# Kernel optimization log

Measured on AMD Instinct MI355X. Metric: run time of the kernel, lower is better.

Reference implementation:

```python
import jax, jax.numpy as jnp
import numpy as np

MUL = 32      # multiplicity of each irrep type: 32x0e + 32x1o (dim = 32 + 96 = 128)
NSPEC = 10
NGRAPH = 16
EPS = 1e-5


def _split(x):
    # x: [N, 128] -> scalars [N, 32], vectors [N, 32, 3]
    return x[:, :MUL], x[:, MUL:].reshape(x.shape[0], MUL, 3)


def _cat(s, v):
    return jnp.concatenate([s, v.reshape(v.shape[0], MUL * 3)], axis=1)


def _irreps_linear(s, v, w0, w1, b0=None):
    # e3nn o3.Linear: per-irrep-type multiplicity mixing, /sqrt(fan_in), bias on scalars only
    inv = 1.0 / np.sqrt(MUL)
    s2 = s @ w0 * inv
    if b0 is not None:
        s2 = s2 + b0
    v2 = jnp.einsum('nuc,uw->nwc', v, w1) * inv
    return s2, v2


def _tensor_product(s1, v1, s2, v2, w000, w110, w011, w101):
    # SeparateWeightTensorProduct with per-path internal weights, lmax=1 paths:
    #   0e x 0e -> 0e, 1o x 1o -> 0e (CG = delta/sqrt(3)), 0e x 1o -> 1o, 1o x 0e -> 1o
    inv = 1.0 / np.sqrt(MUL * MUL)
    half = 1.0 / np.sqrt(2.0)  # two paths feed each output irrep
    out0 = (jnp.einsum('nu,nv,uvw->nw', s1, s2, w000)
            + jnp.einsum('nuc,nvc,uvw->nw', v1, v2, w110) / np.sqrt(3.0)) * (inv * half)
    out1 = (jnp.einsum('nu,nvc,uvw->nwc', s1, v2, w011)
            + jnp.einsum('nuc,nv,uvw->nwc', v1, s2, w101)) * (inv * half)
    return out0, out1


def _e3_layer_norm(s, v, batch, ln_w0, ln_b0, ln_w1):
    # per-graph equivariant layer norm: subtract mean on scalars, RMS-normalize each irrep field
    ones = jnp.ones(batch.shape, s.dtype)
    cnt = jnp.maximum(jax.ops.segment_sum(ones, batch, NGRAPH), 1.0)
    mean = jax.ops.segment_sum(s.sum(-1), batch, NGRAPH) / (cnt * MUL)
    s = s - mean[batch][:, None]
    n2s = jax.ops.segment_sum((s * s).sum(-1), batch, NGRAPH) / (cnt * MUL)
    s = s * jax.lax.rsqrt(n2s + EPS)[batch][:, None] * ln_w0 + ln_b0
    n2v = jax.ops.segment_sum((v * v).sum((-1, -2)), batch, NGRAPH) / (cnt * MUL)
    v = v * jax.lax.rsqrt(n2v + EPS)[batch][:, None, None] * ln_w1[None, :, None]
    return s, v


def setup_inputs() -> dict:
    key = jax.random.key(0)
    ks = jax.random.split(key, 24)
    N, B = 50000, 2
    rn = lambda k, sh: jax.random.normal(k, sh, dtype=jnp.float32)
    inp = {
        'node_feats_hidden': rn(ks[0], (B, N, MUL * 4)),
        'node_feats_up': rn(ks[1], (N, MUL * 4)),
        'hl_w0': rn(ks[2], (B, MUL, MUL)), 'hl_w1': rn(ks[3], (B, MUL, MUL)),
        'ul_w0': rn(ks[4], (B, MUL, MUL)), 'ul_w1': rn(ks[5], (B, MUL, MUL)),
        'tp_w000': rn(ks[6], (B, MUL, MUL, MUL)), 'tp_w110': rn(ks[7], (B, MUL, MUL, MUL)),
        'tp_w011': rn(ks[8], (B, MUL, MUL, MUL)), 'tp_w101': rn(ks[9], (B, MUL, MUL, MUL)),
        'lp_w0': rn(ks[10], (B, MUL, MUL)), 'lp_b0': jnp.zeros((B, MUL), jnp.float32),
        'lp_w1': rn(ks[11], (B, MUL, MUL)),
        'sc_w0': rn(ks[12], (B, MUL, NSPEC, MUL)), 'sc_w1': rn(ks[13], (B, MUL, NSPEC, MUL)),
        'ln_w0': jnp.ones((B, MUL), jnp.float32), 'ln_b0': jnp.zeros((B, MUL), jnp.float32),
        'ln_w1': jnp.ones((B, MUL), jnp.float32),
        'sk_w0': rn(ks[14], (B, MUL, MUL)), 'sk_b0': jnp.zeros((B, MUL), jnp.float32),
        'sk_w1': rn(ks[15], (B, MUL, MUL)),
        'node_species': jax.random.randint(ks[16], (N,), 0, NSPEC),
        'batch': jnp.sort(jax.random.randint(ks[17], (N,), 0, NGRAPH)),
    }
    return inp


def reference(node_feats_hidden, node_feats_up, hl_w0, hl_w1, ul_w0, ul_w1,
              tp_w000, tp_w110, tp_w011, tp_w101, lp_w0, lp_b0, lp_w1,
              sc_w0, sc_w1, ln_w0, ln_b0, ln_w1, sk_w0, sk_b0, sk_w1,
              node_species, batch):
    oh = jax.nn.one_hot(node_species, NSPEC, dtype=node_feats_up.dtype)
    inv_sc = 1.0 / np.sqrt(MUL * NSPEC)
    up = node_feats_up
    outs = []
    for b in range(node_feats_hidden.shape[0]):  # num_interactions blocks (fixed, small)
        sh, vh = _split(node_feats_hidden[b])
        su, vu = _split(up)
        shp, vhp = _irreps_linear(sh, vh, hl_w0[b], hl_w1[b])
        sup, vup = _irreps_linear(su, vu, ul_w0[b], ul_w1[b])
        z0, z1 = _tensor_product(shp, vhp, sup, vup,
                                 tp_w000[b], tp_w110[b], tp_w011[b], tp_w101[b])
        z0, z1 = _irreps_linear(z0, z1, lp_w0[b], lp_w1[b], lp_b0[b])
        # self connection: FullyConnectedTensorProduct(hidden, one-hot '10x0e', out)
        z0 = z0 + jnp.einsum('nu,nv,uvw->nw', sh, oh, sc_w0[b]) * inv_sc
        z1 = z1 + jnp.einsum('nuc,nv,uvw->nwc', vh, oh, sc_w1[b]) * inv_sc
        z0, z1 = _e3_layer_norm(z0, z1, batch, ln_w0[b], ln_b0[b], ln_w1[b])
        sk0, sk1 = _irreps_linear(sh, vh, sk_w0[b], sk_w1[b], sk_b0[b])
        out = _cat(z0 + sk0, z1 + sk1)
        outs.append(out)
        up = out  # next block consumes this block's output as node_feats_up
    return jnp.stack(outs)
```

## Files before the change

### kernel.cpp

```cpp
#include <hip/hip_runtime.h>
#include <math.h>

#define MULT 32
#define NSPEC 10
#define NGRAPH 16
#define NBANK 64
#define NCBANK 16
#define INV_SC 0.05590169943749474f
#define INV32S 0.17677669529663687f

typedef unsigned short u16;
typedef __bf16 v8bf __attribute__((ext_vector_type(8)));
typedef float v4f __attribute__((ext_vector_type(4)));
typedef unsigned int v4u_t __attribute__((ext_vector_type(4)));

__device__ __forceinline__ u16 f2bf(float f) {
    unsigned int u = __builtin_bit_cast(unsigned int, f);
    unsigned int r = u + 0x7fffu + ((u >> 16) & 1u);
    return (u16)(r >> 16);
}

__device__ __forceinline__ v8bf frag16(const u16* p) {
    return __builtin_bit_cast(v8bf, *(const v4u_t*)p);
}

#define MFMA(a, b, c) __builtin_amdgcn_mfma_f32_16x16x32_bf16(a, b, c, 0, 0, 0)

__global__ void zero_kernel(float* __restrict__ p, int n) {
    int i = blockIdx.x * 256 + threadIdx.x;
    if (i < n) p[i] = 0.0f;
}

__global__ void count_kernel(const int* __restrict__ batch, float* __restrict__ cntb, int N) {
    __shared__ int bins[NGRAPH];
    int t = threadIdx.x;
    if (t < NGRAPH) bins[t] = 0;
    __syncthreads();
    int i = blockIdx.x * 256 + t;
    if (i < N) atomicAdd(&bins[batch[i]], 1);
    __syncthreads();
    int bank = blockIdx.x & (NCBANK - 1);
    if (t < NGRAPH && bins[t] > 0) atomicAdd(&cntb[bank * NGRAPH + t], (float)bins[t]);
}

__global__ void stageA_kernel(const float* __restrict__ w000, const float* __restrict__ w110,
                              const float* __restrict__ w011, const float* __restrict__ w101,
                              const float* __restrict__ lp0, const float* __restrict__ lp1,
                              float* __restrict__ tmp1) {
    int gid = blockIdx.x * 256 + threadIdx.x;
    int tslot = gid >> 15;
    int e = gid & 32767;
    int z = e & 31;
    int uv = e >> 5;
    int b = tslot >> 2, path = tslot & 3;
    const float* W = (path == 0 ? w000 : path == 1 ? w110 : path == 2 ? w011 : w101) + b * 32768;
    const float* L = ((path == 0 || path == 1) ? lp0 : lp1) + b * 1024;
    float scale = (path == 1) ? (1.0f / (8192.0f * 1.7320508075688772f)) : (1.0f / 8192.0f);
    const float* wr = W + uv * 32;
    float acc = 0.0f;
    for (int w = 0; w < 32; ++w) acc += wr[w] * L[w * 32 + z];
    tmp1[gid] = acc * scale;
}

__global__ void stageB_kernel(const float* __restrict__ ul0, const float* __restrict__ ul1,
                              const float* __restrict__ tmp1, float* __restrict__ tmp2) {
    int gid = blockIdx.x * 256 + threadIdx.x;
    int tslot = gid >> 15;
    int e = gid & 32767;
    int z = e & 31;
    int bb = (e >> 5) & 31;
    int u = e >> 10;
    int b = tslot >> 2, path = tslot & 3;
    const float* U = ((path == 0 || path == 3) ? ul0 : ul1) + b * 1024;
    const float* in = tmp1 + (size_t)tslot * 32768 + u * 1024 + z;
    float acc = 0.0f;
    for (int v = 0; v < 32; ++v) acc += U[bb * 32 + v] * in[v * 32];
    tmp2[gid] = acc;
}

__global__ void stageC_kernel(const float* __restrict__ hl0, const float* __restrict__ hl1,
                              const float* __restrict__ tmp2, float* __restrict__ Weff) {
    int gid = blockIdx.x * 256 + threadIdx.x;
    int tslot = gid >> 15;
    int e = gid & 32767;
    int z = e & 31;
    int bb = (e >> 5) & 31;
    int a = e >> 10;
    int b = tslot >> 2, path = tslot & 3;
    const float* H = ((path == 0 || path == 2) ? hl0 : hl1) + b * 1024;
    const float* in = tmp2 + (size_t)tslot * 32768 + bb * 32 + z;
    float acc = 0.0f;
    for (int u = 0; u < 32; ++u) acc += H[a * 32 + u] * in[u * 1024];
    Weff[gid] = acc;
}

__global__ void pack_kernel(const float* __restrict__ Weff,
                            const float* __restrict__ sc_w0, const float* __restrict__ sc_w1,
                            u16* __restrict__ packs, int total) {
    int gid = blockIdx.x * 256 + threadIdx.x;
    if (gid >= total) return;
    int b = gid / 151552;
    int e = gid - b * 151552;
    float v;
    if (e < 131072) {
        int which = e >> 15;
        int e2 = e & 32767;
        int k = e2 & 31;
        int z = (e2 >> 5) & 31;
        int hi = e2 >> 10;
        int path = (which == 0) ? 0 : (which == 1) ? 2 : (which == 2) ? 3 : 1;
        int a  = (which < 2) ? k  : hi;
        int bb = (which < 2) ? hi : k;
        v = Weff[(size_t)((b * 4 + path) * 32 + a) * 1024 + bb * 32 + z];
    } else {
        int e2 = e - 131072;
        int which = e2 / 10240;
        int e3 = e2 - which * 10240;
        int s = e3 >> 10, z = (e3 >> 5) & 31, a = e3 & 31;
        const float* S = which ? sc_w1 : sc_w0;
        v = S[(size_t)b * 10240 + a * 320 + s * 32 + z] * INV_SC;
    }
    packs[gid] = f2bf(v);
}

__attribute__((amdgpu_waves_per_eu(4, 4)))
__global__ __launch_bounds__(256)
void tp_kernel(const float* __restrict__ hidden_b, const float* __restrict__ up,
               const u16* __restrict__ pk,
               const float* __restrict__ lp_b0,
               const int* __restrict__ species, const int* __restrict__ batch,
               float* __restrict__ S1b, float* __restrict__ S2b, float* __restrict__ V2b,
               float* __restrict__ zout, int N) {
    constexpr int OFF_000 = 0, OFF_011 = 32768, OFF_101 = 65536, OFF_110 = 98304;
    constexpr int OFF_SC0 = 131072, OFF_SC1 = 141312;

    __shared__ __align__(16) char smem[33792];
    __shared__ int spec_l[16];
    __shared__ int bat_l[16];
    __shared__ float gs1[NGRAPH], gs2[NGRAPH], gv2[NGRAPH];

    u16* sh_bf = (u16*)smem;
    u16* su_bf = (u16*)(smem + 1280);
    u16* vu_bf = (u16*)(smem + 2560);
    u16* vh_bf = (u16*)(smem + 6400);
    float* suT = (float*)(smem + 10240);
    float* vuT = (float*)(smem + 12288);
    float* vhT = (float*)(smem + 18432);
    float* red = (float*)smem;

    const int t = threadIdx.x;
    const int w = t >> 6, lane = t & 63, quad = lane >> 4, c16 = lane & 15;
    const int n0 = blockIdx.x * 16;
    const int nvalid = min(16, N - n0);

    if (t < NGRAPH) { gs1[t] = 0.f; gs2[t] = 0.f; gv2[t] = 0.f; }
    if (t < 16) {
        spec_l[t] = (t < nvalid) ? species[n0 + t] : -1;
        bat_l[t]  = (t < nvalid) ? batch[n0 + t] : 0;
    }
    for (int i = t; i < 2048; i += 256) {
        int n = i >> 7, col = i & 127;
        float hv = 0.f, uv = 0.f;
        if (n < nvalid) {
            hv = hidden_b[(size_t)(n0 + n) * 128 + col];
            uv = up[(size_t)(n0 + n) * 128 + col];
        }
        if (col < 32) {
            sh_bf[n * 40 + col] = f2bf(hv); su_bf[n * 40 + col] = f2bf(uv);
            suT[col * 16 + n] = uv;
        } else {
            int idx = col - 32, c = idx % 3, a = idx / 3;
            vh_bf[(c * 16 + n) * 40 + a] = f2bf(hv);
            vu_bf[(c * 16 + n) * 40 + a] = f2bf(uv);
            vhT[(c * 32 + a) * 16 + n] = hv;
            vuT[(c * 32 + a) * 16 + n] = uv;
        }
    }
    __syncthreads();

    const v4f z4 = {0.f, 0.f, 0.f, 0.f};
    v4f o0[2];
    v4f o1[3][2];
    o0[0] = z4; o0[1] = z4;
#pragma unroll
    for (int c = 0; c < 3; ++c) { o1[c][0] = z4; o1[c][1] = z4; }

    v8bf a_sh = frag16(sh_bf + c16 * 40 + quad * 8);

    {
        const u16* Wb = pk + OFF_000 + (w * 16 * 16 + c16) * 32 + quad * 8;
#pragma unroll 4
        for (int th = 0; th < 8; ++th) {
            int bb = w * 8 + th;
            v4f y = *(const v4f*)(suT + bb * 16 + quad * 4);
            v8bf bf0 = frag16(Wb + (th * 2) * 512);
            v8bf bf1 = frag16(Wb + (th * 2 + 1) * 512);
            v4f C0 = MFMA(a_sh, bf0, z4);
            v4f C1 = MFMA(a_sh, bf1, z4);
#pragma unroll
            for (int r = 0; r < 4; ++r) {
                o0[0][r] += C0[r] * y[r];
                o0[1][r] += C1[r] * y[r];
            }
        }
    }
    {
        const u16* Wb = pk + OFF_011 + (w * 16 * 16 + c16) * 32 + quad * 8;
#pragma unroll 2
        for (int th = 0; th < 8; ++th) {
            int bb = w * 8 + th;
            v8bf bf0 = frag16(Wb + (th * 2) * 512);
            v8bf bf1 = frag16(Wb + (th * 2 + 1) * 512);
            v4f C0 = MFMA(a_sh, bf0, z4);
            v4f C1 = MFMA(a_sh, bf1, z4);
#pragma unroll
            for (int c = 0; c < 3; ++c) {
                v4f y = *(const v4f*)(vuT + (c * 32 + bb) * 16 + quad * 4);
#pragma unroll
                for (int r = 0; r < 4; ++r) {
                    o1[c][0][r] += C0[r] * y[r];
                    o1[c][1][r] += C1[r] * y[r];
                }
            }
        }
    }
    {
        v8bf a_su = frag16(su_bf + c16 * 40 + quad * 8);
        const u16* Wb = pk + OFF_101 + (w * 16 * 16 + c16) * 32 + quad * 8;
#pragma unroll 2
        for (int th = 0; th < 8; ++th) {
            int aa = w * 8 + th;
            v8bf bf0 = frag16(Wb + (th * 2) * 512);
            v8bf bf1 = frag16(Wb + (th * 2 + 1) * 512);
            v4f C0 = MFMA(a_su, bf0, z4);
            v4f C1 = MFMA(a_su, bf1, z4);
#pragma unroll
            for (int c = 0; c < 3; ++c) {
                v4f y = *(const v4f*)(vhT + (c * 32 + aa) * 16 + quad * 4);
#pragma unroll
                for (int r = 0; r < 4; ++r) {
                    o1[c][0][r] += C0[r] * y[r];
                    o1[c][1][r] += C1[r] * y[r];
                }
            }
        }
    }
#pragma unroll
    for (int c = 0; c < 3; ++c) {
        v8bf av = frag16(vu_bf + (c * 16 + c16) * 40 + quad * 8);
        const u16* Wb = pk + OFF_110 + (w * 16 * 16 + c16) * 32 + quad * 8;
#pragma unroll 4
        for (int th = 0; th < 8; ++th) {
            int aa = w * 8 + th;
            v4f y = *(const v4f*)(vhT + (c * 32 + aa) * 16 + quad * 4);
            v8bf bf0 = frag16(Wb + (th * 2) * 512);
            v8bf bf1 = frag16(Wb + (th * 2 + 1) * 512);
            v4f C0 = MFMA(av, bf0, z4);
            v4f C1 = MFMA(av, bf1, z4);
#pragma unroll
            for (int r = 0; r < 4; ++r) {
                o0[0][r] += C0[r] * y[r];
                o0[1][r] += C1[r] * y[r];
            }
        }
    }
    {
        const int s0 = (w < 2) ? w * 3 : 6 + (w - 2) * 2;
        const int ns = (w < 2) ? 3 : 2;
        v8bf zf = __builtin_bit_cast(v8bf, (v4u_t){0u, 0u, 0u, 0u});
        int sp = spec_l[c16];
        for (int si = s0; si < s0 + ns; ++si) {
            bool m = (sp == si);
            v8bf ash_m = m ? a_sh : zf;
#pragma unroll
            for (int zh = 0; zh < 2; ++zh) {
                int boff = (si * 32 + zh * 16 + c16) * 32 + quad * 8;
                v8bf bf0 = frag16(pk + OFF_SC0 + boff);
                v8bf bf1 = frag16(pk + OFF_SC1 + boff);
                o0[zh] = MFMA(ash_m, bf0, o0[zh]);
#pragma unroll
                for (int c = 0; c < 3; ++c) {
                    v8bf av = frag16(vh_bf + (c * 16 + c16) * 40 + quad * 8);
                    v8bf am = m ? av : zf;
                    o1[c][zh] = MFMA(am, bf1, o1[c][zh]);
                }
            }
        }
    }

    __syncthreads();
#pragma unroll
    for (int r = 0; r < 4; ++r) {
        int n = quad * 4 + r;
        float* row = red + (w * 16 + n) * 132;
        row[c16]      = o0[0][r];
        row[16 + c16] = o0[1][r];
#pragma unroll
        for (int c = 0; c < 3; ++c) {
            row[32 + c16 * 3 + c]        = o1[c][0][r];
            row[32 + (16 + c16) * 3 + c] = o1[c][1][r];
        }
    }
    __syncthreads();
    {
        int n = t >> 4, seg = t & 15;
        v4f sa = z4, sb = z4;
#pragma unroll
        for (int ww = 0; ww < 4; ++ww) {
            const float* rp = red + (ww * 16 + n) * 132 + seg * 8;
            sa += *(const v4f*)rp;
            sb += *(const v4f*)(rp + 4);
        }
        float s1p = 0.f, s2p = 0.f, v2p = 0.f;
        if (seg < 4) {
            sa += *(const v4f*)(lp_b0 + seg * 8);
            sb += *(const v4f*)(lp_b0 + seg * 8 + 4);
            s1p = sa[0] + sa[1] + sa[2] + sa[3] + sb[0] + sb[1] + sb[2] + sb[3];
            s2p = sa[0]*sa[0] + sa[1]*sa[1] + sa[2]*sa[2] + sa[3]*sa[3]
                + sb[0]*sb[0] + sb[1]*sb[1] + sb[2]*sb[2] + sb[3]*sb[3];
        } else {
            v2p = sa[0]*sa[0] + sa[1]*sa[1] + sa[2]*sa[2] + sa[3]*sa[3]
                + sb[0]*sb[0] + sb[1]*sb[1] + sb[2]*sb[2] + sb[3]*sb[3];
        }
        if (n < nvalid) {
            float* op = zout + (size_t)(n0 + n) * 128 + seg * 8;
            *(v4f*)op = sa;
            *(v4f*)(op + 4) = sb;
        }
#pragma unroll
        for (int off = 8; off >= 1; off >>= 1) {
            s1p += __shfl_xor(s1p, off, 16);
            s2p += __shfl_xor(s2p, off, 16);
            v2p += __shfl_xor(v2p, off, 16);
        }
        if (seg == 0 && n < nvalid) {
            int g = bat_l[n];
            atomicAdd(&gs1[g], s1p);
            atomicAdd(&gs2[g], s2p);
            atomicAdd(&gv2[g], v2p);
        }
    }
    __syncthreads();
    {
        const int bank = blockIdx.x & (NBANK - 1);
        if (t < NGRAPH) {
            if (gs1[t] != 0.f) atomicAdd(&S1b[bank * NGRAPH + t], gs1[t]);
            if (gs2[t] != 0.f) atomicAdd(&S2b[bank * NGRAPH + t], gs2[t]);
            if (gv2[t] != 0.f) atomicAdd(&V2b[bank * NGRAPH + t], gv2[t]);
        }
    }
}

__global__ __launch_bounds__(256)
void norm_kernel(const float* __restrict__ hidden_b, float* __restrict__ out_b,
                 const float* __restrict__ skw0, const float* __restrict__ skb0,
                 const float* __restrict__ skw1,
                 const float* __restrict__ lnw0, const float* __restrict__ lnb0,
                 const float* __restrict__ lnw1,
                 const int* __restrict__ batch,
                 const float* __restrict__ S1b, const float* __restrict__ S2b,
                 const float* __restrict__ V2b, const float* __restrict__ cntb, int N) {
    __shared__ __align__(16) float sh_l[8][32];
    __shared__ __align__(16) float vh_l[8][96];
    __shared__ float stat_s[3][NGRAPH];
    __shared__ float cnt_s[NGRAPH];
    const int t = threadIdx.x, z = t & 31, nl = t >> 5;
    const int n0 = blockIdx.x * 8;
    for (int i = t; i < 8 * 128; i += 256) {
        int n = i >> 7, col = i & 127;
        float v = (n0 + n < N) ? hidden_b[(size_t)(n0 + n) * 128 + col] : 0.f;
        if (col < 32) sh_l[n][col] = v; else vh_l[n][col - 32] = v;
    }
    if (t < 48) {
        int arr = t >> 4, g = t & 15;
        const float* base = (arr == 0) ? S1b : (arr == 1) ? S2b : V2b;
        float s = 0.f;
        for (int k = 0; k < NBANK; ++k) s += base[k * NGRAPH + g];
        stat_s[arr][g] = s;
    } else if (t < 64) {
        int g = t - 48;
        float c = 0.f;
        for (int k = 0; k < NCBANK; ++k) c += cntb[k * NGRAPH + g];
        cnt_s[g] = c;
    }
    __syncthreads();
    const int n = n0 + nl;
    if (n >= N) return;

    float sk0 = 0.f, s1 = 0.f, s2 = 0.f, s3 = 0.f;
    for (int a = 0; a < 32; ++a) {
        float w0 = skw0[a * 32 + z];
        float w1 = skw1[a * 32 + z];
        sk0 += sh_l[nl][a] * w0;
        s1 += vh_l[nl][a * 3 + 0] * w1;
        s2 += vh_l[nl][a * 3 + 1] * w1;
        s3 += vh_l[nl][a * 3 + 2] * w1;
    }
    int g = batch[n];
    float cM = fmaxf(cnt_s[g], 1.0f) * 32.0f;
    float mean = stat_s[0][g] / cM;
    float var = fmaxf(stat_s[1][g] / cM - mean * mean, 0.0f);
    float rs = rsqrtf(var + 1e-5f);
    float rv = rsqrtf(fmaxf(stat_s[2][g] / cM, 0.0f) + 1e-5f);

    size_t base = (size_t)n * 128;
    float z0 = out_b[base + z];
    out_b[base + z] = (z0 - mean) * rs * lnw0[z] + lnb0[z] + sk0 * INV32S + skb0[z];
    float lw = lnw1[z] * rv;
    float x0 = out_b[base + 32 + z * 3 + 0];
    float x1 = out_b[base + 32 + z * 3 + 1];
    float x2 = out_b[base + 32 + z * 3 + 2];
    out_b[base + 32 + z * 3 + 0] = x0 * lw + s1 * INV32S;
    out_b[base + 32 + z * 3 + 1] = x1 * lw + s2 * INV32S;
    out_b[base + 32 + z * 3 + 2] = x2 * lw + s3 * INV32S;
}

extern "C" void kernel_launch(void* const* d_in, const int* in_sizes, int n_in,
                              void* d_out, int out_size, void* d_ws, size_t ws_size,
                              hipStream_t stream) {
    const float* hidden = (const float*)d_in[0];
    const float* up0    = (const float*)d_in[1];
    const float* hl_w0  = (const float*)d_in[2];
    const float* hl_w1  = (const float*)d_in[3];
    const float* ul_w0  = (const float*)d_in[4];
    const float* ul_w1  = (const float*)d_in[5];
    const float* w000   = (const float*)d_in[6];
    const float* w110   = (const float*)d_in[7];
    const float* w011   = (const float*)d_in[8];
    const float* w101   = (const float*)d_in[9];
    const float* lp_w0  = (const float*)d_in[10];
    const float* lp_b0  = (const float*)d_in[11];
    const float* lp_w1  = (const float*)d_in[12];
    const float* sc_w0  = (const float*)d_in[13];
    const float* sc_w1  = (const float*)d_in[14];
    const float* ln_w0  = (const float*)d_in[15];
    const float* ln_b0  = (const float*)d_in[16];
    const float* ln_w1  = (const float*)d_in[17];
    const float* sk_w0  = (const float*)d_in[18];
    const float* sk_b0  = (const float*)d_in[19];
    const float* sk_w1  = (const float*)d_in[20];
    const int* species  = (const int*)d_in[21];
    const int* batch    = (const int*)d_in[22];
    float* out = (float*)d_out;

    const int N = in_sizes[21];
    const int B = in_sizes[0] / (N * 128);

    float* ws = (float*)d_ws;
    float* tmp1 = ws;
    float* tmp2 = tmp1 + (size_t)B * 4 * 32768;
    float* cntb = tmp2 + (size_t)B * 4 * 32768;
    float* S1b = cntb + NCBANK * NGRAPH;
    float* S2b = S1b + (size_t)B * NBANK * NGRAPH;
    float* V2b = S2b + (size_t)B * NBANK * NGRAPH;
    int statn = NCBANK * NGRAPH + 3 * B * NBANK * NGRAPH;

    zero_kernel<<<(statn + 255) / 256, 256, 0, stream>>>(cntb, statn);
    count_kernel<<<(N + 255) / 256, 256, 0, stream>>>(batch, cntb, N);

    int nb = B * 4 * 32768 / 256;
    stageA_kernel<<<nb, 256, 0, stream>>>(w000, w110, w011, w101, lp_w0, lp_w1, tmp1);
    stageB_kernel<<<nb, 256, 0, stream>>>(ul_w0, ul_w1, tmp1, tmp2);
    stageC_kernel<<<nb, 256, 0, stream>>>(hl_w0, hl_w1, tmp2, tmp1);

    u16* packs = (u16*)tmp2;
    int ptotal = B * 151552;
    pack_kernel<<<(ptotal + 255) / 256, 256, 0, stream>>>(tmp1, sc_w0, sc_w1, packs, ptotal);

    for (int b = 0; b < B; ++b) {
        const float* up = (b == 0) ? up0 : out + (size_t)(b - 1) * N * 128;
        const u16* pb = packs + (size_t)b * 151552;
        tp_kernel<<<(N + 15) / 16, 256, 0, stream>>>(
            hidden + (size_t)b * N * 128, up, pb,
            lp_b0 + b * MULT, species, batch,
            S1b + (size_t)b * NBANK * NGRAPH, S2b + (size_t)b * NBANK * NGRAPH,
            V2b + (size_t)b * NBANK * NGRAPH,
            out + (size_t)b * N * 128, N);
        norm_kernel<<<(N + 7) / 8, 256, 0, stream>>>(
            hidden + (size_t)b * N * 128, out + (size_t)b * N * 128,
            sk_w0 + b * 1024, sk_b0 + b * MULT, sk_w1 + b * 1024,
            ln_w0 + b * MULT, ln_b0 + b * MULT, ln_w1 + b * MULT,
            batch, S1b + (size_t)b * NBANK * NGRAPH, S2b + (size_t)b * NBANK * NGRAPH,
            V2b + (size_t)b * NBANK * NGRAPH, cntb, N);
    }
}
```

Before: 409.4 us.

## Retile tensor-product kernel to 64 nodes per block with LDS-staged weights

The tp_kernel now handles 64 nodes per block, one 16-node tile per wave, instead of splitting a 16-node tile's output dimension across four waves. Each weight chunk is double-buffered into LDS with global_load_lds and shared by all four waves, so weight traffic per node drops and the cross-wave reduction through LDS goes away. The pack layout is changed to match the per-lane fragment order, and the self-connection loop skips species with no nodes in the wave. In exchange the LDS footprint grows, the per-thread register load is larger, and the kernel relies on hand-written vmcnt waits and barriers.

```diff
diff --git a/kernel.cpp b/kernel.cpp
--- a/kernel.cpp
+++ b/kernel.cpp
@@ -6,6 +6,7 @@
 #define NGRAPH 16
 #define NBANK 64
 #define NCBANK 16
+#define NCHUNK 32
 #define INV_SC 0.05590169943749474f
 #define INV32S 0.17677669529663687f
 
@@ -25,6 +26,10 @@
 }
 
 #define MFMA(a, b, c) __builtin_amdgcn_mfma_f32_16x16x32_bf16(a, b, c, 0, 0, 0)
+
+#define GLL(g, l) __builtin_amdgcn_global_load_lds( \
+    (const __attribute__((address_space(1))) unsigned int*)(g), \
+    (__attribute__((address_space(3))) unsigned int*)(l), 16, 0, 0)
 
 __global__ void zero_kernel(float* __restrict__ p, int n) {
     int i = blockIdx.x * 256 + threadIdx.x;
@@ -105,9 +110,13 @@
     if (e < 131072) {
         int which = e >> 15;
         int e2 = e & 32767;
-        int k = e2 & 31;
-        int z = (e2 >> 5) & 31;
-        int hi = e2 >> 10;
+        int g = e2 >> 9;
+        int off = e2 & 511;
+        int lane = off >> 3, j = off & 7;
+        int c16v = lane & 15, quadv = lane >> 4;
+        int k = quadv * 8 + j;
+        int z = (g & 1) * 16 + c16v;
+        int hi = g >> 1;
         int path = (which == 0) ? 0 : (which == 1) ? 2 : (which == 2) ? 3 : 1;
         int a  = (which < 2) ? k  : hi;
         int bb = (which < 2) ? hi : k;
@@ -123,218 +132,241 @@
     packs[gid] = f2bf(v);
 }
 
-__attribute__((amdgpu_waves_per_eu(4, 4)))
-__global__ __launch_bounds__(256)
+__global__ __launch_bounds__(256, 2)
 void tp_kernel(const float* __restrict__ hidden_b, const float* __restrict__ up,
                const u16* __restrict__ pk,
                const float* __restrict__ lp_b0,
                const int* __restrict__ species, const int* __restrict__ batch,
                float* __restrict__ S1b, float* __restrict__ S2b, float* __restrict__ V2b,
                float* __restrict__ zout, int N) {
-    constexpr int OFF_000 = 0, OFF_011 = 32768, OFF_101 = 65536, OFF_110 = 98304;
-    constexpr int OFF_SC0 = 131072, OFF_SC1 = 141312;
-
-    __shared__ __align__(16) char smem[33792];
-    __shared__ int spec_l[16];
-    __shared__ int bat_l[16];
+    __shared__ __align__(16) float ybuf[14336];
+    __shared__ __align__(16) u16 wbuf[2][4096];
     __shared__ float gs1[NGRAPH], gs2[NGRAPH], gv2[NGRAPH];
 
-    u16* sh_bf = (u16*)smem;
-    u16* su_bf = (u16*)(smem + 1280);
-    u16* vu_bf = (u16*)(smem + 2560);
-    u16* vh_bf = (u16*)(smem + 6400);
-    float* suT = (float*)(smem + 10240);
-    float* vuT = (float*)(smem + 12288);
-    float* vhT = (float*)(smem + 18432);
-    float* red = (float*)smem;
+    float* yS = ybuf;
+    float* yV = ybuf + 2048;
+    float* yH = ybuf + 8192;
 
     const int t = threadIdx.x;
-    const int w = t >> 6, lane = t & 63, quad = lane >> 4, c16 = lane & 15;
-    const int n0 = blockIdx.x * 16;
-    const int nvalid = min(16, N - n0);
+    const int wv = t >> 6, lane = t & 63, quad = lane >> 4, c16 = lane & 15;
+    const int n0 = blockIdx.x * 64;
+    const int nvalid = min(64, N - n0);
+    const u16* wsrc = pk;
+    const u16* pkSC0 = pk + 131072;
+    const u16* pkSC1 = pk + 141312;
+
+#define STAGE(ch, bf) do { \
+        const u16* gsrc_ = wsrc + (ch) * 4096 + wv * 1024 + lane * 8; \
+        GLL(gsrc_, &wbuf[bf][wv * 1024]); \
+        GLL(gsrc_ + 512, &wbuf[bf][wv * 1024 + 512]); \
+    } while (0)
+
+    STAGE(0, 0);
+    STAGE(1, 1);
 
     if (t < NGRAPH) { gs1[t] = 0.f; gs2[t] = 0.f; gv2[t] = 0.f; }
-    if (t < 16) {
-        spec_l[t] = (t < nvalid) ? species[n0 + t] : -1;
-        bat_l[t]  = (t < nvalid) ? batch[n0 + t] : 0;
-    }
-    for (int i = t; i < 2048; i += 256) {
-        int n = i >> 7, col = i & 127;
-        float hv = 0.f, uv = 0.f;
-        if (n < nvalid) {
-            hv = hidden_b[(size_t)(n0 + n) * 128 + col];
-            uv = up[(size_t)(n0 + n) * 128 + col];
-        }
-        if (col < 32) {
-            sh_bf[n * 40 + col] = f2bf(hv); su_bf[n * 40 + col] = f2bf(uv);
-            suT[col * 16 + n] = uv;
+
+    const int myloc = wv * 16 + c16;
+    const bool av_ok = myloc < nvalid;
+    const int myn = n0 + (av_ok ? myloc : 0);
+    int sp = -1;
+    v8bf a_sh, a_su, a_vh[3], a_vu[3];
+    const v8bf zf = __builtin_bit_cast(v8bf, (v4u_t){0u, 0u, 0u, 0u});
+    {
+        const float* hrow = hidden_b + (size_t)myn * 128;
+        const float* urow = up + (size_t)myn * 128;
+        v4f h0 = *(const v4f*)(hrow + quad * 8), h1 = *(const v4f*)(hrow + quad * 8 + 4);
+        v4f u0 = *(const v4f*)(urow + quad * 8), u1 = *(const v4f*)(urow + quad * 8 + 4);
+        v4u_t ws, wu;
+#pragma unroll
+        for (int k = 0; k < 2; ++k) {
+            ws[k]     = f2bf(h0[2*k]) | ((unsigned)f2bf(h0[2*k+1]) << 16);
+            ws[k + 2] = f2bf(h1[2*k]) | ((unsigned)f2bf(h1[2*k+1]) << 16);
+            wu[k]     = f2bf(u0[2*k]) | ((unsigned)f2bf(u0[2*k+1]) << 16);
+            wu[k + 2] = f2bf(u1[2*k]) | ((unsigned)f2bf(u1[2*k+1]) << 16);
+        }
+        a_sh = __builtin_bit_cast(v8bf, ws);
+        a_su = __builtin_bit_cast(v8bf, wu);
+        float hv24[24], uv24[24];
+#pragma unroll
+        for (int q2 = 0; q2 < 6; ++q2) {
+            v4f hv = *(const v4f*)(hrow + 32 + quad * 24 + q2 * 4);
+            v4f uv = *(const v4f*)(urow + 32 + quad * 24 + q2 * 4);
+#pragma unroll
+            for (int jj = 0; jj < 4; ++jj) { hv24[q2*4+jj] = hv[jj]; uv24[q2*4+jj] = uv[jj]; }
+        }
+#pragma unroll
+        for (int c = 0; c < 3; ++c) {
+            v4u_t wh, wv2;
+#pragma unroll
+            for (int k = 0; k < 4; ++k) {
+                wh[k]  = f2bf(hv24[(2*k)*3 + c]) | ((unsigned)f2bf(hv24[(2*k+1)*3 + c]) << 16);
+                wv2[k] = f2bf(uv24[(2*k)*3 + c]) | ((unsigned)f2bf(uv24[(2*k+1)*3 + c]) << 16);
+            }
+            a_vh[c] = __builtin_bit_cast(v8bf, wh);
+            a_vu[c] = __builtin_bit_cast(v8bf, wv2);
+        }
+        if (!av_ok) {
+            a_sh = zf; a_su = zf;
+#pragma unroll
+            for (int c = 0; c < 3; ++c) { a_vh[c] = zf; a_vu[c] = zf; }
         } else {
-            int idx = col - 32, c = idx % 3, a = idx / 3;
-            vh_bf[(c * 16 + n) * 40 + a] = f2bf(hv);
-            vu_bf[(c * 16 + n) * 40 + a] = f2bf(uv);
-            vhT[(c * 32 + a) * 16 + n] = hv;
-            vuT[(c * 32 + a) * 16 + n] = uv;
+            sp = species[myn];
+        }
+    }
+
+    {
+        const int nl = t & 63, cc = t >> 6;
+        const bool nok = nl < nvalid;
+        const float* hr = hidden_b + (size_t)(n0 + (nok ? nl : 0)) * 128 + cc * 32;
+        const float* ur = up + (size_t)(n0 + (nok ? nl : 0)) * 128 + cc * 32;
+        const v4f z4s = {0.f, 0.f, 0.f, 0.f};
+        if (cc == 0) {
+#pragma unroll
+            for (int j4 = 0; j4 < 8; ++j4) {
+                v4f uv = nok ? *(const v4f*)(ur + j4 * 4) : z4s;
+#pragma unroll
+                for (int jj = 0; jj < 4; ++jj) yS[(j4 * 4 + jj) * 64 + nl] = uv[jj];
+            }
+        } else {
+#pragma unroll
+            for (int j4 = 0; j4 < 8; ++j4) {
+                v4f hv = nok ? *(const v4f*)(hr + j4 * 4) : z4s;
+                v4f uv = nok ? *(const v4f*)(ur + j4 * 4) : z4s;
+#pragma unroll
+                for (int jj = 0; jj < 4; ++jj) {
+                    int idx = (cc - 1) * 32 + j4 * 4 + jj;
+                    int a = (idx * 171) >> 9;
+                    int c = idx - a * 3;
+                    yV[(c * 32 + a) * 64 + nl] = uv[jj];
+                    yH[(c * 32 + a) * 64 + nl] = hv[jj];
+                }
+            }
         }
     }
     __syncthreads();
 
     const v4f z4 = {0.f, 0.f, 0.f, 0.f};
+    const int yb = wv * 16 + quad * 4;
     v4f o0[2];
     v4f o1[3][2];
     o0[0] = z4; o0[1] = z4;
 #pragma unroll
     for (int c = 0; c < 3; ++c) { o1[c][0] = z4; o1[c][1] = z4; }
 
-    v8bf a_sh = frag16(sh_bf + c16 * 40 + quad * 8);
+#define RD_WF(bf, pr) \
+    v8bf wf0 = frag16(&wbuf[bf][(pr) * 1024 + lane * 8]); \
+    v8bf wf1 = frag16(&wbuf[bf][(pr) * 1024 + 512 + lane * 8]);
+
+#define BODY_000 { RD_WF(buf, pr) \
+    v4f y = *(const v4f*)(yS + hi * 64 + yb); \
+    v4f C0 = MFMA(a_sh, wf0, z4); v4f C1 = MFMA(a_sh, wf1, z4); \
+    _Pragma("unroll") for (int r = 0; r < 4; ++r) { o0[0][r] += C0[r] * y[r]; o0[1][r] += C1[r] * y[r]; } }
+
+#define BODY_011 { RD_WF(buf, pr) \
+    v4f C0 = MFMA(a_sh, wf0, z4); v4f C1 = MFMA(a_sh, wf1, z4); \
+    _Pragma("unroll") for (int c = 0; c < 3; ++c) { \
+        v4f y = *(const v4f*)(yV + (c * 32 + hi) * 64 + yb); \
+        _Pragma("unroll") for (int r = 0; r < 4; ++r) { o1[c][0][r] += C0[r] * y[r]; o1[c][1][r] += C1[r] * y[r]; } } }
+
+#define BODY_101 { RD_WF(buf, pr) \
+    v4f C0 = MFMA(a_su, wf0, z4); v4f C1 = MFMA(a_su, wf1, z4); \
+    _Pragma("unroll") for (int c = 0; c < 3; ++c) { \
+        v4f y = *(const v4f*)(yH + (c * 32 + hi) * 64 + yb); \
+        _Pragma("unroll") for (int r = 0; r < 4; ++r) { o1[c][0][r] += C0[r] * y[r]; o1[c][1][r] += C1[r] * y[r]; } } }
+
+#define BODY_110 { RD_WF(buf, pr) \
+    _Pragma("unroll") for (int c = 0; c < 3; ++c) { \
+        v4f y = *(const v4f*)(yH + (c * 32 + hi) * 64 + yb); \
+        v4f C0 = MFMA(a_vu[c], wf0, z4); v4f C1 = MFMA(a_vu[c], wf1, z4); \
+        _Pragma("unroll") for (int r = 0; r < 4; ++r) { o0[0][r] += C0[r] * y[r]; o0[1][r] += C1[r] * y[r]; } } }
+
+#define SECTION(SEC, WAITASM, BODY) \
+    for (int c8 = 0; c8 < 8; ++c8) { \
+        const int ch = (SEC) * 8 + c8; \
+        const int buf = ch & 1; \
+        asm volatile(WAITASM ::: "memory"); \
+        __builtin_amdgcn_s_barrier(); \
+        _Pragma("unroll") \
+        for (int pr = 0; pr < 4; ++pr) { \
+            const int hi = c8 * 4 + pr; \
+            BODY \
+        } \
+        __builtin_amdgcn_s_barrier(); \
+        if (ch + 2 < NCHUNK) STAGE(ch + 2, buf); \
+    }
+
+    SECTION(0, "s_waitcnt vmcnt(2)", BODY_000)
+    SECTION(1, "s_waitcnt vmcnt(2)", BODY_011)
+    SECTION(2, "s_waitcnt vmcnt(2)", BODY_101)
+    SECTION(3, "s_waitcnt vmcnt(0)", BODY_110)
 
     {
-        const u16* Wb = pk + OFF_000 + (w * 16 * 16 + c16) * 32 + quad * 8;
-#pragma unroll 4
-        for (int th = 0; th < 8; ++th) {
-            int bb = w * 8 + th;
-            v4f y = *(const v4f*)(suT + bb * 16 + quad * 4);
-            v8bf bf0 = frag16(Wb + (th * 2) * 512);
-            v8bf bf1 = frag16(Wb + (th * 2 + 1) * 512);
-            v4f C0 = MFMA(a_sh, bf0, z4);
-            v4f C1 = MFMA(a_sh, bf1, z4);
-#pragma unroll
-            for (int r = 0; r < 4; ++r) {
-                o0[0][r] += C0[r] * y[r];
-                o0[1][r] += C1[r] * y[r];
-            }
-        }
-    }
-    {
-        const u16* Wb = pk + OFF_011 + (w * 16 * 16 + c16) * 32 + quad * 8;
-#pragma unroll 2
-        for (int th = 0; th < 8; ++th) {
-            int bb = w * 8 + th;
-            v8bf bf0 = frag16(Wb + (th * 2) * 512);
-            v8bf bf1 = frag16(Wb + (th * 2 + 1) * 512);
-            v4f C0 = MFMA(a_sh, bf0, z4);
-            v4f C1 = MFMA(a_sh, bf1, z4);
-#pragma unroll
-            for (int c = 0; c < 3; ++c) {
-                v4f y = *(const v4f*)(vuT + (c * 32 + bb) * 16 + quad * 4);
-#pragma unroll
-                for (int r = 0; r < 4; ++r) {
-                    o1[c][0][r] += C0[r] * y[r];
-                    o1[c][1][r] += C1[r] * y[r];
+#pragma unroll 1
+        for (int si = 0; si < NSPEC; ++si) {
+            if (__any(sp == si)) {
+                bool m = (sp == si);
+                v8bf ash_m = m ? a_sh : zf;
+#pragma unroll
+                for (int zh = 0; zh < 2; ++zh) {
+                    int boff = (si * 32 + zh * 16 + c16) * 32 + quad * 8;
+                    v8bf bf0 = frag16(pkSC0 + boff);
+                    v8bf bf1 = frag16(pkSC1 + boff);
+                    o0[zh] = MFMA(ash_m, bf0, o0[zh]);
+#pragma unroll
+                    for (int c = 0; c < 3; ++c) {
+                        v8bf am = m ? a_vh[c] : zf;
+                        o1[c][zh] = MFMA(am, bf1, o1[c][zh]);
+                    }
                 }
             }
         }
     }
+
     {
-        v8bf a_su = frag16(su_bf + c16 * 40 + quad * 8);
-        const u16* Wb = pk + OFF_101 + (w * 16 * 16 + c16) * 32 + quad * 8;
-#pragma unroll 2
-        for (int th = 0; th < 8; ++th) {
-            int aa = w * 8 + th;
-            v8bf bf0 = frag16(Wb + (th * 2) * 512);
-            v8bf bf1 = frag16(Wb + (th * 2 + 1) * 512);
-            v4f C0 = MFMA(a_su, bf0, z4);
-            v4f C1 = MFMA(a_su, bf1, z4);
+        float bias0 = lp_b0[c16], bias1 = lp_b0[16 + c16];
+        float* row_base = ybuf + wv * 2112;
+#pragma unroll
+        for (int r = 0; r < 4; ++r) {
+            int n = quad * 4 + r;
+            float* row = row_base + n * 132;
+            row[c16]      = o0[0][r] + bias0;
+            row[16 + c16] = o0[1][r] + bias1;
 #pragma unroll
             for (int c = 0; c < 3; ++c) {
-                v4f y = *(const v4f*)(vhT + (c * 32 + aa) * 16 + quad * 4);
-#pragma unroll
-                for (int r = 0; r < 4; ++r) {
-                    o1[c][0][r] += C0[r] * y[r];
-                    o1[c][1][r] += C1[r] * y[r];
-                }
+                row[32 + c16 * 3 + c]        = o1[c][0][r];
+                row[32 + (16 + c16) * 3 + c] = o1[c][1][r];
             }
         }
-    }
-#pragma unroll
-    for (int c = 0; c < 3; ++c) {
-        v8bf av = frag16(vu_bf + (c * 16 + c16) * 40 + quad * 8);
-        const u16* Wb = pk + OFF_110 + (w * 16 * 16 + c16) * 32 + quad * 8;
-#pragma unroll 4
-        for (int th = 0; th < 8; ++th) {
-            int aa = w * 8 + th;
-            v4f y = *(const v4f*)(vhT + (c * 32 + aa) * 16 + quad * 4);
-            v8bf bf0 = frag16(Wb + (th * 2) * 512);
-            v8bf bf1 = frag16(Wb + (th * 2 + 1) * 512);
-            v4f C0 = MFMA(av, bf0, z4);
-            v4f C1 = MFMA(av, bf1, z4);
-#pragma unroll
-            for (int r = 0; r < 4; ++r) {
-                o0[0][r] += C0[r] * y[r];
-                o0[1][r] += C1[r] * y[r];
-            }
-        }
-    }
-    {
-        const int s0 = (w < 2) ? w * 3 : 6 + (w - 2) * 2;
-        const int ns = (w < 2) ? 3 : 2;
-        v8bf zf = __builtin_bit_cast(v8bf, (v4u_t){0u, 0u, 0u, 0u});
-        int sp = spec_l[c16];
-        for (int si = s0; si < s0 + ns; ++si) {
-            bool m = (sp == si);
-            v8bf ash_m = m ? a_sh : zf;
-#pragma unroll
-            for (int zh = 0; zh < 2; ++zh) {
-                int boff = (si * 32 + zh * 16 + c16) * 32 + quad * 8;
-                v8bf bf0 = frag16(pk + OFF_SC0 + boff);
-                v8bf bf1 = frag16(pk + OFF_SC1 + boff);
-                o0[zh] = MFMA(ash_m, bf0, o0[zh]);
-#pragma unroll
-                for (int c = 0; c < 3; ++c) {
-                    v8bf av = frag16(vh_bf + (c * 16 + c16) * 40 + quad * 8);
-                    v8bf am = m ? av : zf;
-                    o1[c][zh] = MFMA(am, bf1, o1[c][zh]);
-                }
-            }
-        }
-    }
-
-    __syncthreads();
-#pragma unroll
-    for (int r = 0; r < 4; ++r) {
-        int n = quad * 4 + r;
-        float* row = red + (w * 16 + n) * 132;
-        row[c16]      = o0[0][r];
-        row[16 + c16] = o0[1][r];
-#pragma unroll
-        for (int c = 0; c < 3; ++c) {
-            row[32 + c16 * 3 + c]        = o1[c][0][r];
-            row[32 + (16 + c16) * 3 + c] = o1[c][1][r];
-        }
-    }
-    __syncthreads();
-    {
-        int n = t >> 4, seg = t & 15;
-        v4f sa = z4, sb = z4;
-#pragma unroll
-        for (int ww = 0; ww < 4; ++ww) {
-            const float* rp = red + (ww * 16 + n) * 132 + seg * 8;
-            sa += *(const v4f*)rp;
-            sb += *(const v4f*)(rp + 4);
+        int rr = lane >> 2, seg = lane & 3;
+        const float* rp = row_base + rr * 132 + seg * 32;
+        v4f sa[8];
+#pragma unroll
+        for (int k = 0; k < 8; ++k) sa[k] = *(const v4f*)(rp + k * 4);
+        const int gn = n0 + wv * 16 + rr;
+        const bool ok = (wv * 16 + rr) < nvalid;
+        if (ok) {
+            float* op = zout + (size_t)gn * 128 + seg * 32;
+#pragma unroll
+            for (int k = 0; k < 8; ++k) *(v4f*)(op + k * 4) = sa[k];
         }
         float s1p = 0.f, s2p = 0.f, v2p = 0.f;
-        if (seg < 4) {
-            sa += *(const v4f*)(lp_b0 + seg * 8);
-            sb += *(const v4f*)(lp_b0 + seg * 8 + 4);
-            s1p = sa[0] + sa[1] + sa[2] + sa[3] + sb[0] + sb[1] + sb[2] + sb[3];
-            s2p = sa[0]*sa[0] + sa[1]*sa[1] + sa[2]*sa[2] + sa[3]*sa[3]
-                + sb[0]*sb[0] + sb[1]*sb[1] + sb[2]*sb[2] + sb[3]*sb[3];
+        if (seg == 0) {
+#pragma unroll
+            for (int k = 0; k < 8; ++k)
+#pragma unroll
+                for (int jj = 0; jj < 4; ++jj) { s1p += sa[k][jj]; s2p += sa[k][jj] * sa[k][jj]; }
         } else {
-            v2p = sa[0]*sa[0] + sa[1]*sa[1] + sa[2]*sa[2] + sa[3]*sa[3]
-                + sb[0]*sb[0] + sb[1]*sb[1] + sb[2]*sb[2] + sb[3]*sb[3];
-        }
-        if (n < nvalid) {
-            float* op = zout + (size_t)(n0 + n) * 128 + seg * 8;
-            *(v4f*)op = sa;
-            *(v4f*)(op + 4) = sb;
-        }
-#pragma unroll
-        for (int off = 8; off >= 1; off >>= 1) {
-            s1p += __shfl_xor(s1p, off, 16);
-            s2p += __shfl_xor(s2p, off, 16);
-            v2p += __shfl_xor(v2p, off, 16);
-        }
-        if (seg == 0 && n < nvalid) {
-            int g = bat_l[n];
+#pragma unroll
+            for (int k = 0; k < 8; ++k)
+#pragma unroll
+                for (int jj = 0; jj < 4; ++jj) v2p += sa[k][jj] * sa[k][jj];
+        }
+        s1p += __shfl_xor(s1p, 1, 4); s1p += __shfl_xor(s1p, 2, 4);
+        s2p += __shfl_xor(s2p, 1, 4); s2p += __shfl_xor(s2p, 2, 4);
+        v2p += __shfl_xor(v2p, 1, 4); v2p += __shfl_xor(v2p, 2, 4);
+        if (seg == 0 && ok) {
+            int g = batch[gn];
             atomicAdd(&gs1[g], s1p);
             atomicAdd(&gs2[g], s2p);
             atomicAdd(&gv2[g], v2p);
@@ -349,6 +381,13 @@
             if (gv2[t] != 0.f) atomicAdd(&V2b[bank * NGRAPH + t], gv2[t]);
         }
     }
+#undef STAGE
+#undef RD_WF
+#undef BODY_000
+#undef BODY_011
+#undef BODY_101
+#undef BODY_110
+#undef SECTION
 }
 
 __global__ __launch_bounds__(256)
@@ -470,7 +509,7 @@
     for (int b = 0; b < B; ++b) {
         const float* up = (b == 0) ? up0 : out + (size_t)(b - 1) * N * 128;
         const u16* pb = packs + (size_t)b * 151552;
-        tp_kernel<<<(N + 15) / 16, 256, 0, stream>>>(
+        tp_kernel<<<(N + 63) / 64, 256, 0, stream>>>(
             hidden + (size_t)b * N * 128, up, pb,
             lp_b0 + b * MULT, species, batch,
             S1b + (size_t)b * NBANK * NGRAPH, S2b + (size_t)b * NBANK * NGRAPH,
```

After: 1.343 ms. 3.28x slower.

## Halve reduction LDS buffer, fuse 110 channel loop, relax waves-per-EU cap

Applied to the files above, without the earlier changes.

The cross-wave reduction now uses a two-phase accumulate: waves 0-1 write partials, then waves 2-3 add theirs in place. This shrinks the shared buffer from 33792 to 24576 bytes and allows more blocks per CU. The 1o x 1o path now handles all three channel components per weight fragment load, so each B fragment is read once instead of three times. The vh fragments for the self connection are hoisted out of the species loop. The waves-per-EU attribute drops its upper bound. The trade-offs are higher register pressure, an extra barrier, and read-modify-write traffic on shared memory.

```diff
diff --git a/kernel.cpp b/kernel.cpp
--- a/kernel.cpp
+++ b/kernel.cpp
@@ -123,7 +123,7 @@
     packs[gid] = f2bf(v);
 }
 
-__attribute__((amdgpu_waves_per_eu(4, 4)))
+__attribute__((amdgpu_waves_per_eu(4)))
 __global__ __launch_bounds__(256)
 void tp_kernel(const float* __restrict__ hidden_b, const float* __restrict__ up,
                const u16* __restrict__ pk,
@@ -134,7 +134,7 @@
     constexpr int OFF_000 = 0, OFF_011 = 32768, OFF_101 = 65536, OFF_110 = 98304;
     constexpr int OFF_SC0 = 131072, OFF_SC1 = 141312;
 
-    __shared__ __align__(16) char smem[33792];
+    __shared__ __align__(16) char smem[24576];
     __shared__ int spec_l[16];
     __shared__ int bat_l[16];
     __shared__ float gs1[NGRAPH], gs2[NGRAPH], gv2[NGRAPH];
@@ -245,22 +245,26 @@
             }
         }
     }
-#pragma unroll
-    for (int c = 0; c < 3; ++c) {
-        v8bf av = frag16(vu_bf + (c * 16 + c16) * 40 + quad * 8);
+    {
+        v8bf av0 = frag16(vu_bf + (0 * 16 + c16) * 40 + quad * 8);
+        v8bf av1 = frag16(vu_bf + (1 * 16 + c16) * 40 + quad * 8);
+        v8bf av2 = frag16(vu_bf + (2 * 16 + c16) * 40 + quad * 8);
         const u16* Wb = pk + OFF_110 + (w * 16 * 16 + c16) * 32 + quad * 8;
-#pragma unroll 4
+#pragma unroll 2
         for (int th = 0; th < 8; ++th) {
             int aa = w * 8 + th;
-            v4f y = *(const v4f*)(vhT + (c * 32 + aa) * 16 + quad * 4);
             v8bf bf0 = frag16(Wb + (th * 2) * 512);
             v8bf bf1 = frag16(Wb + (th * 2 + 1) * 512);
-            v4f C0 = MFMA(av, bf0, z4);
-            v4f C1 = MFMA(av, bf1, z4);
+            v4f y0 = *(const v4f*)(vhT + (0 * 32 + aa) * 16 + quad * 4);
+            v4f y1 = *(const v4f*)(vhT + (1 * 32 + aa) * 16 + quad * 4);
+            v4f y2 = *(const v4f*)(vhT + (2 * 32 + aa) * 16 + quad * 4);
+            v4f C00 = MFMA(av0, bf0, z4), C01 = MFMA(av0, bf1, z4);
+            v4f C10 = MFMA(av1, bf0, z4), C11 = MFMA(av1, bf1, z4);
+            v4f C20 = MFMA(av2, bf0, z4), C21 = MFMA(av2, bf1, z4);
 #pragma unroll
             for (int r = 0; r < 4; ++r) {
-                o0[0][r] += C0[r] * y[r];
-                o0[1][r] += C1[r] * y[r];
+                o0[0][r] += C00[r] * y0[r] + C10[r] * y1[r] + C20[r] * y2[r];
+                o0[1][r] += C01[r] * y0[r] + C11[r] * y1[r] + C21[r] * y2[r];
             }
         }
     }
@@ -269,36 +273,56 @@
         const int ns = (w < 2) ? 3 : 2;
         v8bf zf = __builtin_bit_cast(v8bf, (v4u_t){0u, 0u, 0u, 0u});
         int sp = spec_l[c16];
+        v8bf a_vh0 = frag16(vh_bf + (0 * 16 + c16) * 40 + quad * 8);
+        v8bf a_vh1 = frag16(vh_bf + (1 * 16 + c16) * 40 + quad * 8);
+        v8bf a_vh2 = frag16(vh_bf + (2 * 16 + c16) * 40 + quad * 8);
         for (int si = s0; si < s0 + ns; ++si) {
             bool m = (sp == si);
             v8bf ash_m = m ? a_sh : zf;
+            v8bf am0 = m ? a_vh0 : zf;
+            v8bf am1 = m ? a_vh1 : zf;
+            v8bf am2 = m ? a_vh2 : zf;
 #pragma unroll
             for (int zh = 0; zh < 2; ++zh) {
                 int boff = (si * 32 + zh * 16 + c16) * 32 + quad * 8;
                 v8bf bf0 = frag16(pk + OFF_SC0 + boff);
                 v8bf bf1 = frag16(pk + OFF_SC1 + boff);
                 o0[zh] = MFMA(ash_m, bf0, o0[zh]);
-#pragma unroll
-                for (int c = 0; c < 3; ++c) {
-                    v8bf av = frag16(vh_bf + (c * 16 + c16) * 40 + quad * 8);
-                    v8bf am = m ? av : zf;
-                    o1[c][zh] = MFMA(am, bf1, o1[c][zh]);
-                }
-            }
-        }
-    }
-
-    __syncthreads();
-#pragma unroll
-    for (int r = 0; r < 4; ++r) {
-        int n = quad * 4 + r;
-        float* row = red + (w * 16 + n) * 132;
-        row[c16]      = o0[0][r];
-        row[16 + c16] = o0[1][r];
-#pragma unroll
-        for (int c = 0; c < 3; ++c) {
-            row[32 + c16 * 3 + c]        = o1[c][0][r];
-            row[32 + (16 + c16) * 3 + c] = o1[c][1][r];
+                o1[0][zh] = MFMA(am0, bf1, o1[0][zh]);
+                o1[1][zh] = MFMA(am1, bf1, o1[1][zh]);
+                o1[2][zh] = MFMA(am2, bf1, o1[2][zh]);
+            }
+        }
+    }
+
+    __syncthreads();
+    if (w < 2) {
+#pragma unroll
+        for (int r = 0; r < 4; ++r) {
+            int n = quad * 4 + r;
+            float* row = red + (w * 16 + n) * 132;
+            row[c16]      = o0[0][r];
+            row[16 + c16] = o0[1][r];
+#pragma unroll
+            for (int c = 0; c < 3; ++c) {
+                row[32 + c16 * 3 + c]        = o1[c][0][r];
+                row[32 + (16 + c16) * 3 + c] = o1[c][1][r];
+            }
+        }
+    }
+    __syncthreads();
+    if (w >= 2) {
+#pragma unroll
+        for (int r = 0; r < 4; ++r) {
+            int n = quad * 4 + r;
+            float* row = red + ((w - 2) * 16 + n) * 132;
+            row[c16]      += o0[0][r];
+            row[16 + c16] += o0[1][r];
+#pragma unroll
+            for (int c = 0; c < 3; ++c) {
+                row[32 + c16 * 3 + c]        += o1[c][0][r];
+                row[32 + (16 + c16) * 3 + c] += o1[c][1][r];
+            }
         }
     }
     __syncthreads();
@@ -306,7 +330,7 @@
         int n = t >> 4, seg = t & 15;
         v4f sa = z4, sb = z4;
 #pragma unroll
-        for (int ww = 0; ww < 4; ++ww) {
+        for (int ww = 0; ww < 2; ++ww) {
             const float* rp = red + (ww * 16 + n) * 132 + seg * 8;
             sa += *(const v4f*)rp;
             sb += *(const v4f*)(rp + 4);
```

Result: faster. 385.2 us (-5.9%).
